# Performance work log

Hardware: AMD Instinct MI355X
Metric: run time of the kernel (lower is better)

## Reference

```python
import jax, jax.numpy as jnp
import numpy as np

WS = 8        # window size (square)
HEADS = 8
DIM = 512
EPS = 1e-5


def _ln(x, g, b):
    m = x.mean(-1, keepdims=True)
    v = x.var(-1, keepdims=True)
    return (x - m) / jnp.sqrt(v + EPS) * g + b


def _bn(x, g, b, m, v):
    # eval-mode BatchNorm2d on NCHW
    sh = (1, -1, 1, 1)
    return (x - m.reshape(sh)) / jnp.sqrt(v.reshape(sh) + EPS) * g.reshape(sh) + b.reshape(sh)


def _win_rev(w, H, W, C):
    # (B*nW, WS*WS, C) -> (B, C, H, W)
    x = w.reshape(-1, H // WS, W // WS, WS, WS, C)
    return x.transpose(0, 5, 1, 3, 2, 4).reshape(-1, C, H, W)


def _win_part(x):
    # (B, C, H, W) -> (B*nW, WS*WS, C)
    B, C, H, W = x.shape
    x = x.reshape(B, C, H // WS, WS, W // WS, WS)
    return x.transpose(0, 2, 4, 3, 5, 1).reshape(-1, WS * WS, C)


def setup_inputs() -> dict:
    key = jax.random.key(0)
    ks = iter(jax.random.split(key, 64))
    def nrm(sh, s=0.02):
        return jax.random.normal(next(ks), sh, jnp.float32) * s
    C, C2, C8 = DIM, DIM // 2, DIM // 8
    B, H, W = 2, 224, 224
    N = WS * WS
    B_ = B * (H // WS) * (W // WS)
    # relative position index (same construction as the torch module)
    coords = np.stack(np.meshgrid(np.arange(WS), np.arange(WS), indexing='ij'))
    cf = coords.reshape(2, -1)
    rel = (cf[:, :, None] - cf[:, None, :]).transpose(1, 2, 0).astype(np.int64)
    rel[:, :, 0] += WS - 1
    rel[:, :, 1] += WS - 1
    rel[:, :, 0] *= 2 * WS - 1
    rel_idx = jnp.asarray(rel.sum(-1), jnp.int32)   # (N, N)
    ones = lambda n: jnp.ones((n,), jnp.float32)
    zeros = lambda n: jnp.zeros((n,), jnp.float32)
    return dict(
        x=jax.random.normal(next(ks), (B_, N, C), jnp.float32),
        w_pa=nrm((C, C2)), b_pa=zeros(C2),
        g_lna=ones(C2) + nrm((C2,), 0.1), b_lna=nrm((C2,), 0.1),
        w_pc=nrm((C, C)), b_pc=zeros(C),
        g_lnc=ones(C) + nrm((C,), 0.1), b_lnc=nrm((C,), 0.1),
        dw_w=nrm((C, 1, 3, 3), 0.1), dw_b=zeros(C),
        g_bn1=ones(C), b_bn1=zeros(C), m_bn1=nrm((C,), 0.1), v_bn1=ones(C),
        ci_w1=nrm((C, C8)), ci_b1=zeros(C8),
        g_bn2=ones(C8), b_bn2=zeros(C8), m_bn2=nrm((C8,), 0.1), v_bn2=ones(C8),
        ci_w2=nrm((C8, C2)), ci_b2=zeros(C2),
        pj_w=nrm((C, C2)), pj_b=zeros(C2),
        g_bn3=ones(C2), b_bn3=zeros(C2), m_bn3=nrm((C2,), 0.1), v_bn3=ones(C2),
        w_qkv=nrm((C2, 3 * C2)), b_qkv=zeros(3 * C2),
        si_w1=nrm((C2, C8)), si_b1=zeros(C8),
        g_bn4=ones(C8), b_bn4=zeros(C8), m_bn4=nrm((C8,), 0.1), v_bn4=ones(C8),
        si_w2=nrm((C8, 1)), si_b2=zeros(1),
        g_lno=ones(C2) + nrm((C2,), 0.1), b_lno=nrm((C2,), 0.1),
        w_out=nrm((C, C)), b_out=zeros(C),
        rpb=nrm(((2 * WS - 1) ** 2, HEADS)),
        rel_idx=rel_idx, H=H, W=W,
    )


def _forward(x, w_pa, b_pa, g_lna, b_lna, w_pc, b_pc, g_lnc, b_lnc,
             dw_w, dw_b, g_bn1, b_bn1, m_bn1, v_bn1,
             ci_w1, ci_b1, g_bn2, b_bn2, m_bn2, v_bn2, ci_w2, ci_b2,
             pj_w, pj_b, g_bn3, b_bn3, m_bn3, v_bn3,
             w_qkv, b_qkv,
             si_w1, si_b1, g_bn4, b_bn4, m_bn4, v_bn4, si_w2, si_b2,
             g_lno, b_lno, w_out, b_out, rpb, rel_idx, H, W):
    B_, N, C = x.shape
    C2 = C // 2
    hd = C2 // HEADS
    scale = hd ** -0.5
    x_att = _ln(x @ w_pa + b_pa, g_lna, b_lna)            # (B_, N, C2)
    x_cnn = _ln(x @ w_pc + b_pc, g_lnc, b_lnc)            # (B_, N, C)
    x_cnn = _win_rev(x_cnn, H, W, C)                      # (B, C, H, W)
    # depthwise 3x3 conv + BN + GELU
    x_cnn = jax.lax.conv_general_dilated(
        x_cnn, dw_w, (1, 1), [(1, 1), (1, 1)],
        feature_group_count=C, dimension_numbers=('NCHW', 'OIHW', 'NCHW')
    ) + dw_b.reshape(1, -1, 1, 1)
    x_cnn = jax.nn.gelu(_bn(x_cnn, g_bn1, b_bn1, m_bn1, v_bn1), approximate=False)
    # channel interaction: global avg pool -> 1x1 conv -> BN -> GELU -> 1x1 conv
    ci = x_cnn.mean((2, 3))                               # (B, C)
    ci = ci @ ci_w1 + ci_b1                               # (B, C/8)
    ci = jax.nn.gelu((ci - m_bn2) / jnp.sqrt(v_bn2 + EPS) * g_bn2 + b_bn2, approximate=False)
    ci = ci @ ci_w2 + ci_b2                               # (B, C2)
    x_cnn = jnp.einsum('bchw,co->bohw', x_cnn, pj_w) + pj_b.reshape(1, -1, 1, 1)  # (B, C2, H, W)
    # windowed multi-head attention
    qkv = (x_att @ w_qkv + b_qkv).reshape(B_, N, 3, HEADS, hd).transpose(2, 0, 3, 1, 4)
    q, k, v = qkv[0], qkv[1], qkv[2]                      # (B_, heads, N, hd)
    B = ci.shape[0]
    gate = jax.nn.sigmoid(ci).reshape(B, 1, HEADS, 1, hd)
    v = (v.reshape(B, -1, HEADS, N, hd) * gate).reshape(B_, HEADS, N, hd)
    attn = jnp.einsum('bhnd,bhmd->bhnm', q * scale, k)    # (B_, heads, N, N)
    bias = rpb[rel_idx[:N, :N].reshape(-1)].reshape(N, N, HEADS).transpose(2, 0, 1)
    attn = jax.nn.softmax(attn + bias[None], axis=-1)
    x_att = jnp.einsum('bhnm,bhmd->bnhd', attn, v).reshape(B_, N, C2)
    # spatial interaction gating of the conv branch
    x_sp = _win_rev(x_att, H, W, C2)                      # (B, C2, H, W)
    si = jnp.einsum('bchw,co->bohw', x_sp, si_w1) + si_b1.reshape(1, -1, 1, 1)
    si = jax.nn.gelu(_bn(si, g_bn4, b_bn4, m_bn4, v_bn4), approximate=False)
    si = jnp.einsum('bchw,co->bohw', si, si_w2) + si_b2.reshape(1, -1, 1, 1)      # (B, 1, H, W)
    x_cnn = _bn(jax.nn.sigmoid(si) * x_cnn, g_bn3, b_bn3, m_bn3, v_bn3)
    x_cnn = _win_part(x_cnn)                              # (B_, N, C2)
    x_att = _ln(x_att, g_lno, b_lno)
    return jnp.concatenate([x_att, x_cnn], axis=-1) @ w_out + b_out


def reference(x, w_pa, b_pa, g_lna, b_lna, w_pc, b_pc, g_lnc, b_lnc,
              dw_w, dw_b, g_bn1, b_bn1, m_bn1, v_bn1,
              ci_w1, ci_b1, g_bn2, b_bn2, m_bn2, v_bn2, ci_w2, ci_b2,
              pj_w, pj_b, g_bn3, b_bn3, m_bn3, v_bn3,
              w_qkv, b_qkv,
              si_w1, si_b1, g_bn4, b_bn4, m_bn4, v_bn4, si_w2, si_b2,
              g_lno, b_lno, w_out, b_out, rpb, rel_idx, H, W):
    return _forward(x, w_pa, b_pa, g_lna, b_lna, w_pc, b_pc, g_lnc, b_lnc,
                    dw_w, dw_b, g_bn1, b_bn1, m_bn1, v_bn1,
                    ci_w1, ci_b1, g_bn2, b_bn2, m_bn2, v_bn2, ci_w2, ci_b2,
                    pj_w, pj_b, g_bn3, b_bn3, m_bn3, v_bn3,
                    w_qkv, b_qkv,
                    si_w1, si_b1, g_bn4, b_bn4, m_bn4, v_bn4, si_w2, si_b2,
                    g_lno, b_lno, w_out, b_out, rpb, rel_idx, H, W)
```

## Files before the change

### kernel.cpp

```cpp
#include <hip/hip_runtime.h>
#include <math.h>

#define EPS 1e-5f
#define MROWS 100352
#define NWIN  1568

typedef __attribute__((ext_vector_type(8))) short bf16x8;
typedef __attribute__((ext_vector_type(4))) float f32x4;

__device__ __forceinline__ unsigned short f2bf(float f) {
  unsigned u = __float_as_uint(f);
  u += 0x7fffu + ((u >> 16) & 1u);
  return (unsigned short)(u >> 16);
}
__device__ __forceinline__ float bf2f(unsigned short s) {
  return __uint_as_float(((unsigned)s) << 16);
}
__device__ __forceinline__ float gelu_exact(float x) {
  return 0.5f * x * (1.f + erff(x * 0.70710678118654752f));
}

#define GLOAD16(gp, lp)                                              \
  __builtin_amdgcn_global_load_lds(                                  \
      (const __attribute__((address_space(1))) void*)(gp),           \
      (__attribute__((address_space(3))) void*)(lp), 16, 0, 0)

__device__ __forceinline__ void stage_half256(
    const unsigned short* __restrict__ base, int r0, int K, int kk,
    unsigned short* lds, int ldsbase, int tid) {
#pragma unroll
  for (int inst = 0; inst < 2; ++inst) {
    int r = inst * 64 + (tid >> 3);
    int cb = ((tid & 7) << 4) ^ ((r & 7) << 4);
    const unsigned short* src = base + (size_t)(r0 + r) * K + kk + (cb >> 1);
    GLOAD16(src, &lds[ldsbase + inst * 4096 + tid * 8]);
  }
}

__device__ __forceinline__ bf16x8 frag_read256(const unsigned short* lds,
                                               int tilebase, int r_t, int cbyte) {
  int off = r_t * 128 + cbyte;
  int phys = off ^ ((r_t & 7) << 4);
  return *(const bf16x8*)&lds[tilebase + (phys >> 1)];
}

template <bool OUTBF>
__global__ __launch_bounds__(512) void gemm256(
    const unsigned short* __restrict__ A, const unsigned short* __restrict__ Bt,
    const float* __restrict__ bias, void* __restrict__ Cout,
    int M, int N, int K) {
  __shared__ unsigned short lds[65536];
  const int tid = threadIdx.x;
  const int lane = tid & 63, wave = tid >> 6;
  const int wr = wave >> 2, wcn = wave & 3;
  int bx, by;
  {
    const int nwg = gridDim.x * gridDim.y;
    int n = blockIdx.y * gridDim.x + blockIdx.x;
    int w = ((nwg & 7) == 0) ? ((n & 7) * (nwg >> 3) + (n >> 3)) : n;
    by = w / gridDim.x;
    bx = w - by * gridDim.x;
  }
  const int row0 = by * 256, col0 = bx * 256;
  const int rl = lane & 15, qd = lane >> 4;
  f32x4 acc[8][4];
#pragma unroll
  for (int m = 0; m < 8; ++m)
#pragma unroll
    for (int n = 0; n < 4; ++n) acc[m][n] = (f32x4){0.f, 0.f, 0.f, 0.f};

  const int KT = K >> 6;
  stage_half256(A, row0, K, 0, lds, 0, tid);
  stage_half256(A, row0 + 128, K, 0, lds, 8192, tid);
  stage_half256(Bt, col0, K, 0, lds, 16384, tid);
  stage_half256(Bt, col0 + 128, K, 0, lds, 24576, tid);

  for (int kt = 0; kt < KT; ++kt) {
    const int b = kt & 1;
    const int abase = b * 32768, bbase = b * 32768 + 16384;
    const int nb = b ^ 1;
    const int kkn = (kt + 1) << 6;
    const bool last = (kt == KT - 1);
    bf16x8 bfr[4][2];
#pragma unroll
    for (int p = 0; p < 4; ++p) {
      if (!last) {
        if (p == 0)      stage_half256(A, row0, K, kkn, lds, nb * 32768, tid);
        else if (p == 1) stage_half256(A, row0 + 128, K, kkn, lds, nb * 32768 + 8192, tid);
        else if (p == 2) stage_half256(Bt, col0, K, kkn, lds, nb * 32768 + 16384, tid);
        else             stage_half256(Bt, col0 + 128, K, kkn, lds, nb * 32768 + 24576, tid);
      }
      if (p == 0) {
        if (!last) asm volatile("s_waitcnt vmcnt(2)" ::: "memory");
        else       asm volatile("s_waitcnt vmcnt(0)" ::: "memory");
      }
      __builtin_amdgcn_s_barrier();
      __builtin_amdgcn_sched_barrier(0);
      if (p == 0) {
#pragma unroll
        for (int n = 0; n < 4; ++n)
#pragma unroll
          for (int ks = 0; ks < 2; ++ks)
            bfr[n][ks] = frag_read256(lds, bbase, wcn * 64 + n * 16 + rl,
                                      ks * 64 + qd * 16);
      }
      bf16x8 af[2][2];
#pragma unroll
      for (int i = 0; i < 2; ++i)
#pragma unroll
        for (int ks = 0; ks < 2; ++ks)
          af[i][ks] = frag_read256(lds, abase, wr * 128 + (2 * p + i) * 16 + rl,
                                   ks * 64 + qd * 16);
      __builtin_amdgcn_s_setprio(1);
#pragma unroll
      for (int i = 0; i < 2; ++i)
#pragma unroll
        for (int n = 0; n < 4; ++n)
#pragma unroll
          for (int ks = 0; ks < 2; ++ks)
            acc[2 * p + i][n] = __builtin_amdgcn_mfma_f32_16x16x32_bf16(
                af[i][ks], bfr[n][ks], acc[2 * p + i][n], 0, 0, 0);
      __builtin_amdgcn_s_setprio(0);
      __builtin_amdgcn_s_barrier();
    }
  }
  const int crow = qd * 4, ccol = rl;
#pragma unroll
  for (int n = 0; n < 4; ++n) {
    const int gc = col0 + wcn * 64 + n * 16 + ccol;
    const float bz = bias[gc];
#pragma unroll
    for (int m = 0; m < 8; ++m) {
      const int gr0 = row0 + wr * 128 + m * 16 + crow;
#pragma unroll
      for (int r = 0; r < 4; ++r) {
        float val = acc[m][n][r] + bz;
        if constexpr (OUTBF)
          ((unsigned short*)Cout)[(size_t)(gr0 + r) * N + gc] = f2bf(val);
        else
          ((float*)Cout)[(size_t)(gr0 + r) * N + gc] = val;
      }
    }
  }
}

__global__ __launch_bounds__(512, 2) void gemm256_f32a(
    const float* __restrict__ A, const unsigned short* __restrict__ Bt,
    const float* __restrict__ bias, unsigned short* __restrict__ Cout,
    int M, int N, int K) {
  __shared__ unsigned short lds[65536];
  const int tid = threadIdx.x;
  const int lane = tid & 63, wave = tid >> 6;
  const int wr = wave >> 2, wcn = wave & 3;
  int bx, by;
  {
    const int nwg = gridDim.x * gridDim.y;
    int n = blockIdx.y * gridDim.x + blockIdx.x;
    int w = ((nwg & 7) == 0) ? ((n & 7) * (nwg >> 3) + (n >> 3)) : n;
    by = w / gridDim.x;
    bx = w - by * gridDim.x;
  }
  const int row0 = by * 256, col0 = bx * 256;
  const int rl = lane & 15, qd = lane >> 4;
  const int arow = tid >> 2;
  const int acg = (tid & 3) << 4;
  f32x4 acc[8][4];
#pragma unroll
  for (int m = 0; m < 8; ++m)
#pragma unroll
    for (int n = 0; n < 4; ++n) acc[m][n] = (f32x4){0.f, 0.f, 0.f, 0.f};

#define LOADA_F32(st, h, kk)                                                   \
  {                                                                            \
    const float* ap = &A[(size_t)(row0 + (h)*128 + arow) * K + (kk) + acg];    \
    st[0] = *(const float4*)(ap);      st[1] = *(const float4*)(ap + 4);       \
    st[2] = *(const float4*)(ap + 8);  st[3] = *(const float4*)(ap + 12);      \
  }
#define WRITEA_BF(st, base)                                                    \
  {                                                                            \
    unsigned q0, q1, q2, q3, q4, q5, q6, q7;                                   \
    asm("v_cvt_pk_bf16_f32 %0, %1, %2" : "=v"(q0) : "v"(st[0].x), "v"(st[0].y)); \
    asm("v_cvt_pk_bf16_f32 %0, %1, %2" : "=v"(q1) : "v"(st[0].z), "v"(st[0].w)); \
    asm("v_cvt_pk_bf16_f32 %0, %1, %2" : "=v"(q2) : "v"(st[1].x), "v"(st[1].y)); \
    asm("v_cvt_pk_bf16_f32 %0, %1, %2" : "=v"(q3) : "v"(st[1].z), "v"(st[1].w)); \
    asm("v_cvt_pk_bf16_f32 %0, %1, %2" : "=v"(q4) : "v"(st[2].x), "v"(st[2].y)); \
    asm("v_cvt_pk_bf16_f32 %0, %1, %2" : "=v"(q5) : "v"(st[2].z), "v"(st[2].w)); \
    asm("v_cvt_pk_bf16_f32 %0, %1, %2" : "=v"(q6) : "v"(st[3].x), "v"(st[3].y)); \
    asm("v_cvt_pk_bf16_f32 %0, %1, %2" : "=v"(q7) : "v"(st[3].z), "v"(st[3].w)); \
    const int sw = (arow & 7) << 4;                                            \
    const int c0 = ((acg << 1)) ^ sw, c1 = ((acg << 1) + 16) ^ sw;             \
    *(uint4*)&lds[(base) + ((arow * 128 + c0) >> 1)] = make_uint4(q0, q1, q2, q3); \
    *(uint4*)&lds[(base) + ((arow * 128 + c1) >> 1)] = make_uint4(q4, q5, q6, q7); \
  }

  const int KT = K >> 6;
  {
    float4 pA0[4], pA1[4];
    LOADA_F32(pA0, 0, 0);
    LOADA_F32(pA1, 1, 0);
    stage_half256(Bt, col0, K, 0, lds, 16384, tid);
    stage_half256(Bt, col0 + 128, K, 0, lds, 24576, tid);
    asm volatile("s_waitcnt vmcnt(4)" ::: "memory");
    WRITEA_BF(pA0, 0);
    WRITEA_BF(pA1, 8192);
    asm volatile("s_waitcnt lgkmcnt(0)" ::: "memory");
  }
  float4 stA0[4], stA1[4];
  for (int kt = 0; kt < KT; ++kt) {
    const int b = kt & 1;
    const int abase = b * 32768, bbase = b * 32768 + 16384;
    const int nb = b ^ 1;
    const int kkn = (kt + 1) << 6;
    const bool last = (kt == KT - 1);
    bf16x8 bfr[4][2];
#pragma unroll
    for (int p = 0; p < 4; ++p) {
      if (p == 0) {
        if (!last) {
          LOADA_F32(stA0, 0, kkn);
          asm volatile("s_waitcnt vmcnt(4)" ::: "memory");
        } else {
          asm volatile("s_waitcnt vmcnt(0)" ::: "memory");
        }
      } else if (p == 1) {
        if (!last) LOADA_F32(stA1, 1, kkn);
      } else if (p == 2) {
        if (!last) {
          stage_half256(Bt, col0, K, kkn, lds, nb * 32768 + 16384, tid);
          asm volatile("s_waitcnt vmcnt(6)" ::: "memory");
          WRITEA_BF(stA0, nb * 32768);
        }
      } else {
        if (!last) {
          stage_half256(Bt, col0 + 128, K, kkn, lds, nb * 32768 + 24576, tid);
          asm volatile("s_waitcnt vmcnt(4)" ::: "memory");
          WRITEA_BF(stA1, nb * 32768 + 8192);
          asm volatile("s_waitcnt lgkmcnt(0)" ::: "memory");
        }
      }
      __builtin_amdgcn_s_barrier();
      __builtin_amdgcn_sched_barrier(0);
      if (p == 0) {
#pragma unroll
        for (int n = 0; n < 4; ++n)
#pragma unroll
          for (int ks = 0; ks < 2; ++ks)
            bfr[n][ks] = frag_read256(lds, bbase, wcn * 64 + n * 16 + rl,
                                      ks * 64 + qd * 16);
      }
      bf16x8 af[2][2];
#pragma unroll
      for (int i = 0; i < 2; ++i)
#pragma unroll
        for (int ks = 0; ks < 2; ++ks)
          af[i][ks] = frag_read256(lds, abase, wr * 128 + (2 * p + i) * 16 + rl,
                                   ks * 64 + qd * 16);
      __builtin_amdgcn_s_setprio(1);
#pragma unroll
      for (int i = 0; i < 2; ++i)
#pragma unroll
        for (int n = 0; n < 4; ++n)
#pragma unroll
          for (int ks = 0; ks < 2; ++ks)
            acc[2 * p + i][n] = __builtin_amdgcn_mfma_f32_16x16x32_bf16(
                af[i][ks], bfr[n][ks], acc[2 * p + i][n], 0, 0, 0);
      __builtin_amdgcn_s_setprio(0);
      __builtin_amdgcn_s_barrier();
    }
  }
#undef LOADA_F32
#undef WRITEA_BF
  const int crow = qd * 4, ccol = rl;
#pragma unroll
  for (int n = 0; n < 4; ++n) {
    const int gc = col0 + wcn * 64 + n * 16 + ccol;
    const float bz = bias[gc];
#pragma unroll
    for (int m = 0; m < 8; ++m) {
      const int gr0 = row0 + wr * 128 + m * 16 + crow;
#pragma unroll
      for (int r = 0; r < 4; ++r)
        Cout[(size_t)(gr0 + r) * N + gc] = f2bf(acc[m][n][r] + bz);
    }
  }
}

__device__ __forceinline__ void wtc(const float* in, unsigned short* out,
                                    int K, int N, int i) {
  if (i < K * N) {
    int n = i / K, k = i - n * K;
    out[i] = f2bf(in[(size_t)k * N + n]);
  }
}

__global__ __launch_bounds__(256) void prep_all(
    const float* __restrict__ w_pa, const float* __restrict__ w_pc,
    const float* __restrict__ pj_w, const float* __restrict__ w_qkv,
    const float* __restrict__ w_out, const float* __restrict__ si_w1,
    const float* __restrict__ b_pa, const float* __restrict__ b_pc,
    const float* __restrict__ rpb, const int* __restrict__ rel,
    unsigned short* __restrict__ WpaT, unsigned short* __restrict__ WpcT,
    unsigned short* __restrict__ PjT, unsigned short* __restrict__ QkvT,
    unsigned short* __restrict__ OutT, unsigned short* __restrict__ SiT,
    float* __restrict__ B12, float* __restrict__ biasf) {
  const int blk = blockIdx.x, t = threadIdx.x;
  if (blk < 512)        wtc(w_pa, WpaT, 512, 256, blk * 256 + t);
  else if (blk < 1536)  wtc(w_pc, WpcT, 512, 512, (blk - 512) * 256 + t);
  else if (blk < 2048)  wtc(pj_w, PjT, 512, 256, (blk - 1536) * 256 + t);
  else if (blk < 2816)  wtc(w_qkv, QkvT, 256, 768, (blk - 2048) * 256 + t);
  else if (blk < 3840)  wtc(w_out, OutT, 512, 512, (blk - 2816) * 256 + t);
  else if (blk < 3904)  wtc(si_w1, SiT, 256, 64, (blk - 3840) * 256 + t);
  else if (blk == 3904) { B12[t] = b_pa[t]; }
  else if (blk < 3907)  { int i = (blk - 3905) * 256 + t; if (i < 512) B12[256 + i] = b_pc[i]; }
  else {
    int i = (blk - 3907) * 256 + t;
    if (i < 4096) {
      int r = rel[i];
#pragma unroll
      for (int h = 0; h < 8; ++h) biasf[h * 4096 + i] = rpb[r * 8 + h];
    }
  }
}

template <int W>
__global__ __launch_bounds__(256) void ln_rows_bf(
    const unsigned short* __restrict__ in, int istride,
    unsigned short* __restrict__ out,
    const float* __restrict__ g, const float* __restrict__ b) {
  const int row = blockIdx.x * 4 + (threadIdx.x >> 6);
  const int t = threadIdx.x & 63;
  constexpr int NE = W / 64;
  float v[NE];
  const size_t ibase = (size_t)row * istride + t * NE;
  const size_t obase = (size_t)row * W + t * NE;
#pragma unroll
  for (int c4 = 0; c4 < NE / 4; ++c4) {
    ushort4 u = *(const ushort4*)&in[ibase + c4 * 4];
    v[c4 * 4 + 0] = bf2f(u.x); v[c4 * 4 + 1] = bf2f(u.y);
    v[c4 * 4 + 2] = bf2f(u.z); v[c4 * 4 + 3] = bf2f(u.w);
  }
  float s = 0.f, sq = 0.f;
#pragma unroll
  for (int j = 0; j < NE; ++j) { s += v[j]; sq += v[j] * v[j]; }
#pragma unroll
  for (int off = 32; off >= 1; off >>= 1) {
    s += __shfl_xor(s, off);
    sq += __shfl_xor(sq, off);
  }
  const float mean = s * (1.f / W);
  const float var = sq * (1.f / W) - mean * mean;
  const float rstd = rsqrtf(var + EPS);
#pragma unroll
  for (int c4 = 0; c4 < NE / 4; ++c4) {
    int c = t * NE + c4 * 4;
    ushort4 o = make_ushort4(
        f2bf((v[c4 * 4 + 0] - mean) * rstd * g[c + 0] + b[c + 0]),
        f2bf((v[c4 * 4 + 1] - mean) * rstd * g[c + 1] + b[c + 1]),
        f2bf((v[c4 * 4 + 2] - mean) * rstd * g[c + 2] + b[c + 2]),
        f2bf((v[c4 * 4 + 3] - mean) * rstd * g[c + 3] + b[c + 3]));
    *(ushort4*)&out[obase + c4 * 4] = o;
  }
}

__global__ __launch_bounds__(256) void dwconv_bn_gelu(
    const unsigned short* __restrict__ xin, const float* __restrict__ wgt9,
    const float* __restrict__ dwb, const float* __restrict__ g1,
    const float* __restrict__ b1, const float* __restrict__ m1,
    const float* __restrict__ v1, unsigned short* __restrict__ outp,
    float* __restrict__ ci_part) {
  __shared__ unsigned short tile[100 * 128];
  __shared__ float psum[8 * 128];
  const int b_ = blockIdx.x;
  const int b = b_ / 784, win = b_ % 784;
  const int wi = win / 28, wj = win % 28;
  const int h0 = wi * 8 - 1, w0 = wj * 8 - 1;
  const int tid = threadIdx.x;
  const int c4 = (tid & 31) * 4;
  const int pg = tid >> 5;
  for (int chunk = 0; chunk < 4; ++chunk) {
    const int c0 = chunk * 128;
    __syncthreads();
#pragma unroll
    for (int it = 0; it < 7; ++it) {
      int idx = it * 256 + tid;
      if (idx < 1600) {
        int p = idx >> 4;
        int ch8 = (idx & 15) * 8;
        int ph = h0 + p / 10, pw = w0 + p % 10;
        uint4 val = {0u, 0u, 0u, 0u};
        if (ph >= 0 && ph < 224 && pw >= 0 && pw < 224) {
          int bs = b * 784 + (ph >> 3) * 28 + (pw >> 3);
          int n = ((ph & 7) << 3) | (pw & 7);
          val = *(const uint4*)&xin[(size_t)(bs * 64 + n) * 512 + c0 + ch8];
        }
        *(uint4*)&tile[p * 128 + ch8] = val;
      }
    }
    __syncthreads();
    float wreg[9][4];
    float scale[4], shift[4], bias0[4];
#pragma unroll
    for (int j = 0; j < 4; ++j) {
      int cc = c0 + c4 + j;
#pragma unroll
      for (int k = 0; k < 9; ++k) wreg[k][j] = wgt9[cc * 9 + k];
      scale[j] = g1[cc] * rsqrtf(v1[cc] + EPS);
      shift[j] = b1[cc] - m1[cc] * scale[j];
      bias0[j] = dwb[cc];
    }
    float cs0 = 0.f, cs1 = 0.f, cs2 = 0.f, cs3 = 0.f;
    for (int q = 0; q < 8; ++q) {
      const int qq = pg * 8 + q;
      const int r = qq >> 3, cc_ = qq & 7;
      float a0 = bias0[0], a1 = bias0[1], a2 = bias0[2], a3 = bias0[3];
#pragma unroll
      for (int dr = 0; dr < 3; ++dr)
#pragma unroll
        for (int dc = 0; dc < 3; ++dc) {
          ushort4 u = *(const ushort4*)&tile[((r + dr) * 10 + cc_ + dc) * 128 + c4];
          const int k = dr * 3 + dc;
          a0 += bf2f(u.x) * wreg[k][0];
          a1 += bf2f(u.y) * wreg[k][1];
          a2 += bf2f(u.z) * wreg[k][2];
          a3 += bf2f(u.w) * wreg[k][3];
        }
      float g0 = gelu_exact(a0 * scale[0] + shift[0]);
      float g1v = gelu_exact(a1 * scale[1] + shift[1]);
      float g2v = gelu_exact(a2 * scale[2] + shift[2]);
      float g3v = gelu_exact(a3 * scale[3] + shift[3]);
      cs0 += g0; cs1 += g1v; cs2 += g2v; cs3 += g3v;
      *(ushort4*)&outp[(size_t)(b_ * 64 + qq) * 512 + c0 + c4] =
          make_ushort4(f2bf(g0), f2bf(g1v), f2bf(g2v), f2bf(g3v));
    }
    *(float4*)&psum[pg * 128 + c4] = make_float4(cs0, cs1, cs2, cs3);
    __syncthreads();
    if (tid < 128) {
      float s = 0.f;
#pragma unroll
      for (int g = 0; g < 8; ++g) s += psum[g * 128 + tid];
      ci_part[(size_t)b_ * 512 + c0 + tid] = s;
    }
  }
}

__global__ __launch_bounds__(512) void ci_reduce(const float* __restrict__ ci_part,
                                                 float* __restrict__ ci_mean) {
  const int b = blockIdx.x, c = threadIdx.x;
  float s = 0.f;
  for (int w = 0; w < 784; ++w) s += ci_part[(size_t)(b * 784 + w) * 512 + c];
  ci_mean[b * 512 + c] = s * (1.f / 50176.f);
}

__global__ __launch_bounds__(512) void ci_gate(
    const float* __restrict__ ci_mean, const float* __restrict__ w1,
    const float* __restrict__ bi1, const float* __restrict__ g2,
    const float* __restrict__ b2, const float* __restrict__ m2,
    const float* __restrict__ v2, const float* __restrict__ w2,
    const float* __restrict__ bi2, float* __restrict__ gate) {
  __shared__ float cm[1024];
  __shared__ float c1[128];
  const int t = threadIdx.x;
  cm[t] = ci_mean[t];
  cm[t + 512] = ci_mean[t + 512];
  __syncthreads();
  if (t < 128) {
    int b = t >> 6, j = t & 63;
    float acc = bi1[j];
    for (int c = 0; c < 512; ++c) acc += cm[b * 512 + c] * w1[c * 64 + j];
    float sc = g2[j] * rsqrtf(v2[j] + EPS);
    c1[t] = gelu_exact((acc - m2[j]) * sc + b2[j]);
  }
  __syncthreads();
  {
    int b = t >> 8, o = t & 255;
    float acc = bi2[o];
#pragma unroll
    for (int j = 0; j < 64; ++j) acc += c1[b * 64 + j] * w2[j * 256 + o];
    gate[b * 256 + o] = 1.f / (1.f + expf(-acc));
  }
}

__global__ __launch_bounds__(256) void attn_si(
    const unsigned short* __restrict__ qkv,
    const unsigned short* __restrict__ xpj,
    const float* __restrict__ gate, const float* __restrict__ biasf,
    const unsigned short* __restrict__ siw1t,
    const float* __restrict__ bi1, const float* __restrict__ g4,
    const float* __restrict__ b4v, const float* __restrict__ m4,
    const float* __restrict__ v4, const float* __restrict__ w2,
    const float* __restrict__ bi2,
    const float* __restrict__ g3, const float* __restrict__ b3v,
    const float* __restrict__ m3, const float* __restrict__ v3,
    const float* __restrict__ glno, const float* __restrict__ blno,
    unsigned short* __restrict__ outc) {
  __shared__ unsigned short smem[26112];
  __shared__ float sig[64];
  const int w = blockIdx.x;
  const int b = w / 784;
  const int tid = threadIdx.x, lane = tid & 63, wave = tid >> 6;
  unsigned short* p_lds = smem + wave * (64 * 68 + 32 * 68);
  unsigned short* vT = p_lds + 64 * 68;
  const int l15 = lane & 15, l4 = lane >> 4;
  const float scale = 0.17677669529663687f;
  f32x4 o0[4][2], o1[4][2];
#pragma unroll
  for (int hh = 0; hh < 2; ++hh) {
    const int h = wave * 2 + hh;
    {
      const float* gh = &gate[b * 256 + h * 32];
      const size_t vbase = ((size_t)w * 64 + lane) * 768 + 512 + h * 32;
#pragma unroll
      for (int c = 0; c < 4; ++c) {
        uint4 vv = *(const uint4*)&qkv[vbase + c * 8];
        float4 gA = *(const float4*)&gh[c * 8];
        float4 gB = *(const float4*)&gh[c * 8 + 4];
        unsigned vw[4] = {vv.x, vv.y, vv.z, vv.w};
        float gg[8] = {gA.x, gA.y, gA.z, gA.w, gB.x, gB.y, gB.z, gB.w};
#pragma unroll
        for (int j = 0; j < 4; ++j) {
          int d = c * 8 + j * 2;
          vT[(d + 0) * 68 + lane] = f2bf(__uint_as_float(vw[j] << 16) * gg[j * 2]);
          vT[(d + 1) * 68 + lane] =
              f2bf(__uint_as_float(vw[j] & 0xffff0000u) * gg[j * 2 + 1]);
        }
      }
    }
    bf16x8 kf[4], qf[4];
    const size_t qkbase = (size_t)w * 64 * 768 + h * 32 + l4 * 8;
#pragma unroll
    for (int t = 0; t < 4; ++t) {
      kf[t] = *(const bf16x8*)&qkv[qkbase + (size_t)(t * 16 + l15) * 768 + 256];
      qf[t] = *(const bf16x8*)&qkv[qkbase + (size_t)(t * 16 + l15) * 768];
    }
    f32x4 s[4][4];
#pragma unroll
    for (int mt = 0; mt < 4; ++mt)
#pragma unroll
      for (int nt = 0; nt < 4; ++nt) s[mt][nt] = (f32x4){0.f, 0.f, 0.f, 0.f};
#pragma unroll
    for (int mt = 0; mt < 4; ++mt)
#pragma unroll
      for (int nt = 0; nt < 4; ++nt)
        s[mt][nt] = __builtin_amdgcn_mfma_f32_16x16x32_bf16(kf[mt], qf[nt],
                                                            s[mt][nt], 0, 0, 0);
    float inv_s[4];
#pragma unroll
    for (int nt = 0; nt < 4; ++nt) {
      float mx = -1e30f;
#pragma unroll
      for (int mt = 0; mt < 4; ++mt) {
        float4 b4 = *(const float4*)&biasf[(h * 64 + nt * 16 + l15) * 64 +
                                           mt * 16 + l4 * 4];
        s[mt][nt][0] = s[mt][nt][0] * scale + b4.x;
        s[mt][nt][1] = s[mt][nt][1] * scale + b4.y;
        s[mt][nt][2] = s[mt][nt][2] * scale + b4.z;
        s[mt][nt][3] = s[mt][nt][3] * scale + b4.w;
#pragma unroll
        for (int r = 0; r < 4; ++r) mx = fmaxf(mx, s[mt][nt][r]);
      }
      mx = fmaxf(mx, __shfl_xor(mx, 16));
      mx = fmaxf(mx, __shfl_xor(mx, 32));
      float sum = 0.f;
#pragma unroll
      for (int mt = 0; mt < 4; ++mt)
#pragma unroll
        for (int r = 0; r < 4; ++r) {
          float e = __expf(s[mt][nt][r] - mx);
          s[mt][nt][r] = e;
          sum += e;
        }
      sum += __shfl_xor(sum, 16);
      sum += __shfl_xor(sum, 32);
      inv_s[nt] = 1.f / sum;
    }
#pragma unroll
    for (int nt = 0; nt < 4; ++nt)
#pragma unroll
      for (int mt = 0; mt < 4; ++mt) {
        ushort4 pk = make_ushort4(f2bf(s[mt][nt][0] * inv_s[nt]),
                                  f2bf(s[mt][nt][1] * inv_s[nt]),
                                  f2bf(s[mt][nt][2] * inv_s[nt]),
                                  f2bf(s[mt][nt][3] * inv_s[nt]));
        *(ushort4*)&p_lds[(nt * 16 + l15) * 68 + mt * 16 + l4 * 4] = pk;
      }
#pragma unroll
    for (int i = 0; i < 4; ++i)
#pragma unroll
      for (int dt = 0; dt < 2; ++dt)
        (hh ? o1 : o0)[i][dt] = (f32x4){0.f, 0.f, 0.f, 0.f};
#pragma unroll
    for (int ks = 0; ks < 2; ++ks) {
      bf16x8 pa[4], vf[2];
#pragma unroll
      for (int i = 0; i < 4; ++i) {
        const unsigned short* pp = &p_lds[(i * 16 + l15) * 68 + ks * 32 + l4 * 8];
        union { bf16x8 v; ushort4 u[2]; } tmp;
        tmp.u[0] = *(const ushort4*)pp;
        tmp.u[1] = *(const ushort4*)(pp + 4);
        pa[i] = tmp.v;
      }
#pragma unroll
      for (int dt = 0; dt < 2; ++dt) {
        const unsigned short* vp = &vT[(dt * 16 + l15) * 68 + ks * 32 + l4 * 8];
        union { bf16x8 v; ushort4 u[2]; } tmp;
        tmp.u[0] = *(const ushort4*)vp;
        tmp.u[1] = *(const ushort4*)(vp + 4);
        vf[dt] = tmp.v;
      }
#pragma unroll
      for (int i = 0; i < 4; ++i)
#pragma unroll
        for (int dt = 0; dt < 2; ++dt)
          (hh ? o1 : o0)[i][dt] = __builtin_amdgcn_mfma_f32_16x16x32_bf16(
              pa[i], vf[dt], (hh ? o1 : o0)[i][dt], 0, 0, 0);
    }
  }
  __syncthreads();
  unsigned short* xattO = smem;
#pragma unroll
  for (int hh = 0; hh < 2; ++hh) {
    const int h = wave * 2 + hh;
#pragma unroll
    for (int i = 0; i < 4; ++i)
#pragma unroll
      for (int dt = 0; dt < 2; ++dt)
#pragma unroll
        for (int r = 0; r < 4; ++r)
          xattO[(i * 16 + l4 * 4 + r) * 264 + h * 32 + dt * 16 + l15] =
              f2bf((hh ? o1 : o0)[i][dt][r]);
  }
  __syncthreads();
  float* s1s = (float*)(smem + 16896);
  {
    f32x4 a4[4];
#pragma unroll
    for (int n = 0; n < 4; ++n) a4[n] = (f32x4){0.f, 0.f, 0.f, 0.f};
#pragma unroll
    for (int ks = 0; ks < 8; ++ks) {
      bf16x8 af = *(const bf16x8*)&xattO[(wave * 16 + l15) * 264 + ks * 32 + l4 * 8];
#pragma unroll
      for (int n = 0; n < 4; ++n) {
        bf16x8 bfr = *(const bf16x8*)&siw1t[(n * 16 + l15) * 256 + ks * 32 + l4 * 8];
        a4[n] = __builtin_amdgcn_mfma_f32_16x16x32_bf16(af, bfr, a4[n], 0, 0, 0);
      }
    }
#pragma unroll
    for (int n = 0; n < 4; ++n) {
      const int j = n * 16 + l15;
      const float sc4 = g4[j] * rsqrtf(v4[j] + EPS);
      const float m4j = m4[j], b4j = b4v[j], bij = bi1[j];
#pragma unroll
      for (int r = 0; r < 4; ++r) {
        float val = (a4[n][r] + bij - m4j) * sc4 + b4j;
        s1s[(wave * 16 + l4 * 4 + r) * 68 + j] = gelu_exact(val);
      }
    }
  }
  __syncthreads();
  if (tid < 64) {
    float a2 = bi2[0];
#pragma unroll
    for (int jj = 0; jj < 64; ++jj) a2 += s1s[tid * 68 + jj] * w2[jj];
    sig[tid] = 1.f / (1.f + expf(-a2));
  }
  __syncthreads();
  {
    const int p = tid >> 2, l = tid & 3;
    float s = 0.f, sq = 0.f;
#pragma unroll
    for (int k = 0; k < 16; ++k) {
      ushort4 u = *(const ushort4*)&xattO[p * 264 + l * 4 + k * 16];
      float x0 = bf2f(u.x), x1 = bf2f(u.y), x2 = bf2f(u.z), x3 = bf2f(u.w);
      s += x0 + x1 + x2 + x3;
      sq += x0 * x0 + x1 * x1 + x2 * x2 + x3 * x3;
    }
    s += __shfl_xor(s, 1);  sq += __shfl_xor(sq, 1);
    s += __shfl_xor(s, 2);  sq += __shfl_xor(sq, 2);
    const float mean = s * (1.f / 256.f);
    const float var = sq * (1.f / 256.f) - mean * mean;
    const float rstd = rsqrtf(var + EPS);
    const size_t orow = ((size_t)w * 64 + p) * 512;
    const float sg = sig[p];
#pragma unroll
    for (int k = 0; k < 16; ++k) {
      const int c = l * 4 + k * 16;
      ushort4 u = *(const ushort4*)&xattO[p * 264 + c];
      *(ushort4*)&outc[orow + c] = make_ushort4(
          f2bf((bf2f(u.x) - mean) * rstd * glno[c + 0] + blno[c + 0]),
          f2bf((bf2f(u.y) - mean) * rstd * glno[c + 1] + blno[c + 1]),
          f2bf((bf2f(u.z) - mean) * rstd * glno[c + 2] + blno[c + 2]),
          f2bf((bf2f(u.w) - mean) * rstd * glno[c + 3] + blno[c + 3]));
      ushort4 pu = *(const ushort4*)&xpj[((size_t)w * 64 + p) * 256 + c];
      float sc0 = g3[c + 0] * rsqrtf(v3[c + 0] + EPS);
      float sc1 = g3[c + 1] * rsqrtf(v3[c + 1] + EPS);
      float sc2 = g3[c + 2] * rsqrtf(v3[c + 2] + EPS);
      float sc3 = g3[c + 3] * rsqrtf(v3[c + 3] + EPS);
      *(ushort4*)&outc[orow + 256 + c] = make_ushort4(
          f2bf(sg * bf2f(pu.x) * sc0 + (b3v[c + 0] - m3[c + 0] * sc0)),
          f2bf(sg * bf2f(pu.y) * sc1 + (b3v[c + 1] - m3[c + 1] * sc1)),
          f2bf(sg * bf2f(pu.z) * sc2 + (b3v[c + 2] - m3[c + 2] * sc2)),
          f2bf(sg * bf2f(pu.w) * sc3 + (b3v[c + 3] - m3[c + 3] * sc3)));
    }
  }
}

extern "C" void kernel_launch(void* const* d_in, const int* in_sizes, int n_in,
                              void* d_out, int out_size, void* d_ws, size_t ws_size,
                              hipStream_t stream) {
  const float* x     = (const float*)d_in[0];
  const float* w_pa  = (const float*)d_in[1];
  const float* b_pa  = (const float*)d_in[2];
  const float* g_lna = (const float*)d_in[3];
  const float* b_lna = (const float*)d_in[4];
  const float* w_pc  = (const float*)d_in[5];
  const float* b_pc  = (const float*)d_in[6];
  const float* g_lnc = (const float*)d_in[7];
  const float* b_lnc = (const float*)d_in[8];
  const float* dw_w  = (const float*)d_in[9];
  const float* dw_b  = (const float*)d_in[10];
  const float* g_bn1 = (const float*)d_in[11];
  const float* b_bn1 = (const float*)d_in[12];
  const float* m_bn1 = (const float*)d_in[13];
  const float* v_bn1 = (const float*)d_in[14];
  const float* ci_w1 = (const float*)d_in[15];
  const float* ci_b1 = (const float*)d_in[16];
  const float* g_bn2 = (const float*)d_in[17];
  const float* b_bn2 = (const float*)d_in[18];
  const float* m_bn2 = (const float*)d_in[19];
  const float* v_bn2 = (const float*)d_in[20];
  const float* ci_w2 = (const float*)d_in[21];
  const float* ci_b2 = (const float*)d_in[22];
  const float* pj_w  = (const float*)d_in[23];
  const float* pj_b  = (const float*)d_in[24];
  const float* g_bn3 = (const float*)d_in[25];
  const float* b_bn3 = (const float*)d_in[26];
  const float* m_bn3 = (const float*)d_in[27];
  const float* v_bn3 = (const float*)d_in[28];
  const float* w_qkv = (const float*)d_in[29];
  const float* b_qkv = (const float*)d_in[30];
  const float* si_w1 = (const float*)d_in[31];
  const float* si_b1 = (const float*)d_in[32];
  const float* g_bn4 = (const float*)d_in[33];
  const float* b_bn4 = (const float*)d_in[34];
  const float* m_bn4 = (const float*)d_in[35];
  const float* v_bn4 = (const float*)d_in[36];
  const float* si_w2 = (const float*)d_in[37];
  const float* si_b2 = (const float*)d_in[38];
  const float* g_lno = (const float*)d_in[39];
  const float* b_lno = (const float*)d_in[40];
  const float* w_out = (const float*)d_in[41];
  const float* b_out = (const float*)d_in[42];
  const float* rpb   = (const float*)d_in[43];
  const int*   rel   = (const int*)d_in[44];

  char* ws = (char*)d_ws;
  unsigned short* G12BF = (unsigned short*)(ws + 0);
  unsigned short* QKVBF = (unsigned short*)(ws + 0);
  unsigned short* A1BF  = (unsigned short*)(ws + 154140672ull);
  unsigned short* C1BF  = (unsigned short*)(ws + 205520896ull);
  unsigned short* CAT   = (unsigned short*)(ws + 205520896ull);
  unsigned short* CVBF  = (unsigned short*)(ws + 308281344ull);
  unsigned short* PJBF  = (unsigned short*)(ws + 411041792ull);
  float*          CIP   = (float*)(ws + 462422016ull);
  float*          CIM   = (float*)(ws + 465633280ull);
  float*          GATE  = (float*)(ws + 465637376ull);
  float*          B12   = (float*)(ws + 465639424ull);
  float*          BIASF = (float*)(ws + 465642496ull);
  unsigned short* WT    = (unsigned short*)(ws + 465773568ull);
  unsigned short* WpaT  = WT + 0;
  unsigned short* WpcT  = WT + 131072;
  unsigned short* PjT   = WT + 393216;
  unsigned short* QkvT  = WT + 524288;
  unsigned short* OutT  = WT + 720896;
  unsigned short* SiT   = WT + 983040;

  const int M = MROWS;
  dim3 b256(256), b512(512);

  prep_all<<<3923, b256, 0, stream>>>(w_pa, w_pc, pj_w, w_qkv, w_out, si_w1,
                                      b_pa, b_pc, rpb, rel,
                                      WpaT, WpcT, PjT, QkvT, OutT, SiT,
                                      B12, BIASF);

  gemm256_f32a<<<dim3(3, M / 256), dim3(512), 0, stream>>>(x, WpaT, B12, G12BF,
                                                           M, 768, 512);
  ln_rows_bf<256><<<M / 4, b256, 0, stream>>>(G12BF, 768, A1BF, g_lna, b_lna);
  ln_rows_bf<512><<<M / 4, b256, 0, stream>>>(G12BF + 256, 768, C1BF, g_lnc, b_lnc);

  dwconv_bn_gelu<<<NWIN, b256, 0, stream>>>(C1BF, dw_w, dw_b, g_bn1, b_bn1, m_bn1,
                                            v_bn1, CVBF, CIP);
  ci_reduce<<<2, b512, 0, stream>>>(CIP, CIM);
  ci_gate<<<1, b512, 0, stream>>>(CIM, ci_w1, ci_b1, g_bn2, b_bn2, m_bn2, v_bn2,
                                  ci_w2, ci_b2, GATE);

  gemm256<true><<<dim3(1, M / 256), dim3(512), 0, stream>>>(CVBF, PjT, pj_b, PJBF,
                                                            M, 256, 512);

  gemm256<true><<<dim3(3, M / 256), dim3(512), 0, stream>>>(A1BF, QkvT, b_qkv, QKVBF,
                                                            M, 768, 256);

  attn_si<<<NWIN, b256, 0, stream>>>(QKVBF, PJBF, GATE, BIASF, SiT,
                                     si_b1, g_bn4, b_bn4, m_bn4, v_bn4,
                                     si_w2, si_b2,
                                     g_bn3, b_bn3, m_bn3, v_bn3,
                                     g_lno, b_lno, CAT);

  gemm256<false><<<dim3(2, M / 256), dim3(512), 0, stream>>>(CAT, OutT, b_out,
                                                             (float*)d_out, M, 512, 512);
}
```

Baseline: 929.7 us.

## Pre-convert input to bf16 for generic GEMM and fuse both LayerNorms into one kernel

Drops the specialized GEMM that read fp32 activations and converted them to bf16 inside its main loop. A separate elementwise kernel now converts x to bf16 once, and the standard bf16 gemm256 consumes it. The two row LayerNorm launches over the same GEMM output are merged into a single kernel that reads each row once and writes both normalized outputs. This trades an extra full pass over x (fp32 read plus bf16 write) for a simpler GEMM pipeline and one fewer LN pass over the intermediate.

```diff
diff --git a/kernel.cpp b/kernel.cpp
--- a/kernel.cpp
+++ b/kernel.cpp
@@ -140,147 +140,6 @@
         else
           ((float*)Cout)[(size_t)(gr0 + r) * N + gc] = val;
       }
-    }
-  }
-}
-
-__global__ __launch_bounds__(512, 2) void gemm256_f32a(
-    const float* __restrict__ A, const unsigned short* __restrict__ Bt,
-    const float* __restrict__ bias, unsigned short* __restrict__ Cout,
-    int M, int N, int K) {
-  __shared__ unsigned short lds[65536];
-  const int tid = threadIdx.x;
-  const int lane = tid & 63, wave = tid >> 6;
-  const int wr = wave >> 2, wcn = wave & 3;
-  int bx, by;
-  {
-    const int nwg = gridDim.x * gridDim.y;
-    int n = blockIdx.y * gridDim.x + blockIdx.x;
-    int w = ((nwg & 7) == 0) ? ((n & 7) * (nwg >> 3) + (n >> 3)) : n;
-    by = w / gridDim.x;
-    bx = w - by * gridDim.x;
-  }
-  const int row0 = by * 256, col0 = bx * 256;
-  const int rl = lane & 15, qd = lane >> 4;
-  const int arow = tid >> 2;
-  const int acg = (tid & 3) << 4;
-  f32x4 acc[8][4];
-#pragma unroll
-  for (int m = 0; m < 8; ++m)
-#pragma unroll
-    for (int n = 0; n < 4; ++n) acc[m][n] = (f32x4){0.f, 0.f, 0.f, 0.f};
-
-#define LOADA_F32(st, h, kk)                                                   \
-  {                                                                            \
-    const float* ap = &A[(size_t)(row0 + (h)*128 + arow) * K + (kk) + acg];    \
-    st[0] = *(const float4*)(ap);      st[1] = *(const float4*)(ap + 4);       \
-    st[2] = *(const float4*)(ap + 8);  st[3] = *(const float4*)(ap + 12);      \
-  }
-#define WRITEA_BF(st, base)                                                    \
-  {                                                                            \
-    unsigned q0, q1, q2, q3, q4, q5, q6, q7;                                   \
-    asm("v_cvt_pk_bf16_f32 %0, %1, %2" : "=v"(q0) : "v"(st[0].x), "v"(st[0].y)); \
-    asm("v_cvt_pk_bf16_f32 %0, %1, %2" : "=v"(q1) : "v"(st[0].z), "v"(st[0].w)); \
-    asm("v_cvt_pk_bf16_f32 %0, %1, %2" : "=v"(q2) : "v"(st[1].x), "v"(st[1].y)); \
-    asm("v_cvt_pk_bf16_f32 %0, %1, %2" : "=v"(q3) : "v"(st[1].z), "v"(st[1].w)); \
-    asm("v_cvt_pk_bf16_f32 %0, %1, %2" : "=v"(q4) : "v"(st[2].x), "v"(st[2].y)); \
-    asm("v_cvt_pk_bf16_f32 %0, %1, %2" : "=v"(q5) : "v"(st[2].z), "v"(st[2].w)); \
-    asm("v_cvt_pk_bf16_f32 %0, %1, %2" : "=v"(q6) : "v"(st[3].x), "v"(st[3].y)); \
-    asm("v_cvt_pk_bf16_f32 %0, %1, %2" : "=v"(q7) : "v"(st[3].z), "v"(st[3].w)); \
-    const int sw = (arow & 7) << 4;                                            \
-    const int c0 = ((acg << 1)) ^ sw, c1 = ((acg << 1) + 16) ^ sw;             \
-    *(uint4*)&lds[(base) + ((arow * 128 + c0) >> 1)] = make_uint4(q0, q1, q2, q3); \
-    *(uint4*)&lds[(base) + ((arow * 128 + c1) >> 1)] = make_uint4(q4, q5, q6, q7); \
-  }
-
-  const int KT = K >> 6;
-  {
-    float4 pA0[4], pA1[4];
-    LOADA_F32(pA0, 0, 0);
-    LOADA_F32(pA1, 1, 0);
-    stage_half256(Bt, col0, K, 0, lds, 16384, tid);
-    stage_half256(Bt, col0 + 128, K, 0, lds, 24576, tid);
-    asm volatile("s_waitcnt vmcnt(4)" ::: "memory");
-    WRITEA_BF(pA0, 0);
-    WRITEA_BF(pA1, 8192);
-    asm volatile("s_waitcnt lgkmcnt(0)" ::: "memory");
-  }
-  float4 stA0[4], stA1[4];
-  for (int kt = 0; kt < KT; ++kt) {
-    const int b = kt & 1;
-    const int abase = b * 32768, bbase = b * 32768 + 16384;
-    const int nb = b ^ 1;
-    const int kkn = (kt + 1) << 6;
-    const bool last = (kt == KT - 1);
-    bf16x8 bfr[4][2];
-#pragma unroll
-    for (int p = 0; p < 4; ++p) {
-      if (p == 0) {
-        if (!last) {
-          LOADA_F32(stA0, 0, kkn);
-          asm volatile("s_waitcnt vmcnt(4)" ::: "memory");
-        } else {
-          asm volatile("s_waitcnt vmcnt(0)" ::: "memory");
-        }
-      } else if (p == 1) {
-        if (!last) LOADA_F32(stA1, 1, kkn);
-      } else if (p == 2) {
-        if (!last) {
-          stage_half256(Bt, col0, K, kkn, lds, nb * 32768 + 16384, tid);
-          asm volatile("s_waitcnt vmcnt(6)" ::: "memory");
-          WRITEA_BF(stA0, nb * 32768);
-        }
-      } else {
-        if (!last) {
-          stage_half256(Bt, col0 + 128, K, kkn, lds, nb * 32768 + 24576, tid);
-          asm volatile("s_waitcnt vmcnt(4)" ::: "memory");
-          WRITEA_BF(stA1, nb * 32768 + 8192);
-          asm volatile("s_waitcnt lgkmcnt(0)" ::: "memory");
-        }
-      }
-      __builtin_amdgcn_s_barrier();
-      __builtin_amdgcn_sched_barrier(0);
-      if (p == 0) {
-#pragma unroll
-        for (int n = 0; n < 4; ++n)
-#pragma unroll
-          for (int ks = 0; ks < 2; ++ks)
-            bfr[n][ks] = frag_read256(lds, bbase, wcn * 64 + n * 16 + rl,
-                                      ks * 64 + qd * 16);
-      }
-      bf16x8 af[2][2];
-#pragma unroll
-      for (int i = 0; i < 2; ++i)
-#pragma unroll
-        for (int ks = 0; ks < 2; ++ks)
-          af[i][ks] = frag_read256(lds, abase, wr * 128 + (2 * p + i) * 16 + rl,
-                                   ks * 64 + qd * 16);
-      __builtin_amdgcn_s_setprio(1);
-#pragma unroll
-      for (int i = 0; i < 2; ++i)
-#pragma unroll
-        for (int n = 0; n < 4; ++n)
-#pragma unroll
-          for (int ks = 0; ks < 2; ++ks)
-            acc[2 * p + i][n] = __builtin_amdgcn_mfma_f32_16x16x32_bf16(
-                af[i][ks], bfr[n][ks], acc[2 * p + i][n], 0, 0, 0);
-      __builtin_amdgcn_s_setprio(0);
-      __builtin_amdgcn_s_barrier();
-    }
-  }
-#undef LOADA_F32
-#undef WRITEA_BF
-  const int crow = qd * 4, ccol = rl;
-#pragma unroll
-  for (int n = 0; n < 4; ++n) {
-    const int gc = col0 + wcn * 64 + n * 16 + ccol;
-    const float bz = bias[gc];
-#pragma unroll
-    for (int m = 0; m < 8; ++m) {
-      const int gr0 = row0 + wr * 128 + m * 16 + crow;
-#pragma unroll
-      for (int r = 0; r < 4; ++r)
-        Cout[(size_t)(gr0 + r) * N + gc] = f2bf(acc[m][n][r] + bz);
     }
   }
 }
@@ -322,43 +181,65 @@
   }
 }
 
-template <int W>
-__global__ __launch_bounds__(256) void ln_rows_bf(
-    const unsigned short* __restrict__ in, int istride,
-    unsigned short* __restrict__ out,
-    const float* __restrict__ g, const float* __restrict__ b) {
+__global__ __launch_bounds__(256) void cvt_bf16(const float* __restrict__ in,
+                                                unsigned short* __restrict__ out,
+                                                int n8) {
+  int i = blockIdx.x * 256 + threadIdx.x;
+  if (i >= n8) return;
+  float4 a = ((const float4*)in)[i * 2];
+  float4 b = ((const float4*)in)[i * 2 + 1];
+  ((ushort4*)out)[i * 2] = make_ushort4(f2bf(a.x), f2bf(a.y), f2bf(a.z), f2bf(a.w));
+  ((ushort4*)out)[i * 2 + 1] = make_ushort4(f2bf(b.x), f2bf(b.y), f2bf(b.z), f2bf(b.w));
+}
+
+__global__ __launch_bounds__(256) void ln_dual(
+    const unsigned short* __restrict__ in,
+    unsigned short* __restrict__ outa,
+    unsigned short* __restrict__ outc,
+    const float* __restrict__ ga, const float* __restrict__ ba,
+    const float* __restrict__ gc, const float* __restrict__ bc) {
   const int row = blockIdx.x * 4 + (threadIdx.x >> 6);
   const int t = threadIdx.x & 63;
-  constexpr int NE = W / 64;
-  float v[NE];
-  const size_t ibase = (size_t)row * istride + t * NE;
-  const size_t obase = (size_t)row * W + t * NE;
-#pragma unroll
-  for (int c4 = 0; c4 < NE / 4; ++c4) {
-    ushort4 u = *(const ushort4*)&in[ibase + c4 * 4];
-    v[c4 * 4 + 0] = bf2f(u.x); v[c4 * 4 + 1] = bf2f(u.y);
-    v[c4 * 4 + 2] = bf2f(u.z); v[c4 * 4 + 3] = bf2f(u.w);
-  }
-  float s = 0.f, sq = 0.f;
-#pragma unroll
-  for (int j = 0; j < NE; ++j) { s += v[j]; sq += v[j] * v[j]; }
+  const size_t ibase = (size_t)row * 768;
+  float va[4], vc[8];
+  {
+    ushort4 u = *(const ushort4*)&in[ibase + t * 4];
+    va[0] = bf2f(u.x); va[1] = bf2f(u.y); va[2] = bf2f(u.z); va[3] = bf2f(u.w);
+    ushort4 u0 = *(const ushort4*)&in[ibase + 256 + t * 8];
+    ushort4 u1 = *(const ushort4*)&in[ibase + 256 + t * 8 + 4];
+    vc[0] = bf2f(u0.x); vc[1] = bf2f(u0.y); vc[2] = bf2f(u0.z); vc[3] = bf2f(u0.w);
+    vc[4] = bf2f(u1.x); vc[5] = bf2f(u1.y); vc[6] = bf2f(u1.z); vc[7] = bf2f(u1.w);
+  }
+  float sa = va[0] + va[1] + va[2] + va[3];
+  float qa = va[0]*va[0] + va[1]*va[1] + va[2]*va[2] + va[3]*va[3];
+  float sc = 0.f, qc = 0.f;
+#pragma unroll
+  for (int j = 0; j < 8; ++j) { sc += vc[j]; qc += vc[j] * vc[j]; }
 #pragma unroll
   for (int off = 32; off >= 1; off >>= 1) {
-    s += __shfl_xor(s, off);
-    sq += __shfl_xor(sq, off);
-  }
-  const float mean = s * (1.f / W);
-  const float var = sq * (1.f / W) - mean * mean;
-  const float rstd = rsqrtf(var + EPS);
-#pragma unroll
-  for (int c4 = 0; c4 < NE / 4; ++c4) {
-    int c = t * NE + c4 * 4;
-    ushort4 o = make_ushort4(
-        f2bf((v[c4 * 4 + 0] - mean) * rstd * g[c + 0] + b[c + 0]),
-        f2bf((v[c4 * 4 + 1] - mean) * rstd * g[c + 1] + b[c + 1]),
-        f2bf((v[c4 * 4 + 2] - mean) * rstd * g[c + 2] + b[c + 2]),
-        f2bf((v[c4 * 4 + 3] - mean) * rstd * g[c + 3] + b[c + 3]));
-    *(ushort4*)&out[obase + c4 * 4] = o;
+    sa += __shfl_xor(sa, off); qa += __shfl_xor(qa, off);
+    sc += __shfl_xor(sc, off); qc += __shfl_xor(qc, off);
+  }
+  const float ma = sa * (1.f / 256.f);
+  const float ra = rsqrtf(qa * (1.f / 256.f) - ma * ma + EPS);
+  const float mc = sc * (1.f / 512.f);
+  const float rc = rsqrtf(qc * (1.f / 512.f) - mc * mc + EPS);
+  {
+    int c = t * 4;
+    *(ushort4*)&outa[(size_t)row * 256 + c] = make_ushort4(
+        f2bf((va[0] - ma) * ra * ga[c + 0] + ba[c + 0]),
+        f2bf((va[1] - ma) * ra * ga[c + 1] + ba[c + 1]),
+        f2bf((va[2] - ma) * ra * ga[c + 2] + ba[c + 2]),
+        f2bf((va[3] - ma) * ra * ga[c + 3] + ba[c + 3]));
+  }
+#pragma unroll
+  for (int half = 0; half < 2; ++half) {
+    int c = t * 8 + half * 4;
+    *(ushort4*)&outc[(size_t)row * 512 + c] = make_ushort4(
+        f2bf((vc[half * 4 + 0] - mc) * rc * gc[c + 0] + bc[c + 0]),
+        f2bf((vc[half * 4 + 1] - mc) * rc * gc[c + 1] + bc[c + 1]),
+        f2bf((vc[half * 4 + 2] - mc) * rc * gc[c + 2] + bc[c + 2]),
+        f2bf((vc[half * 4 + 3] - mc) * rc * gc[c + 3] + bc[c + 3]));
   }
 }
 
@@ -759,6 +640,7 @@
   unsigned short* A1BF  = (unsigned short*)(ws + 154140672ull);
   unsigned short* C1BF  = (unsigned short*)(ws + 205520896ull);
   unsigned short* CAT   = (unsigned short*)(ws + 205520896ull);
+  unsigned short* XBF   = (unsigned short*)(ws + 308281344ull);
   unsigned short* CVBF  = (unsigned short*)(ws + 308281344ull);
   unsigned short* PJBF  = (unsigned short*)(ws + 411041792ull);
   float*          CIP   = (float*)(ws + 462422016ull);
@@ -781,11 +663,11 @@
                                       b_pa, b_pc, rpb, rel,
                                       WpaT, WpcT, PjT, QkvT, OutT, SiT,
                                       B12, BIASF);
-
-  gemm256_f32a<<<dim3(3, M / 256), dim3(512), 0, stream>>>(x, WpaT, B12, G12BF,
-                                                           M, 768, 512);
-  ln_rows_bf<256><<<M / 4, b256, 0, stream>>>(G12BF, 768, A1BF, g_lna, b_lna);
-  ln_rows_bf<512><<<M / 4, b256, 0, stream>>>(G12BF + 256, 768, C1BF, g_lnc, b_lnc);
+  cvt_bf16<<<(M * 512 / 8 + 255) / 256, b256, 0, stream>>>(x, XBF, M * 512 / 8);
+
+  gemm256<true><<<dim3(3, M / 256), dim3(512), 0, stream>>>(XBF, WpaT, B12, G12BF,
+                                                            M, 768, 512);
+  ln_dual<<<M / 4, b256, 0, stream>>>(G12BF, A1BF, C1BF, g_lna, b_lna, g_lnc, b_lnc);
 
   dwconv_bn_gelu<<<NWIN, b256, 0, stream>>>(C1BF, dw_w, dw_b, g_bn1, b_bn1, m_bn1,
                                             v_bn1, CVBF, CIP);
```

New measurement: 816.4 us (median of 2 runs). -12.2%, faster.
